# Performance work log

Hardware: AMD Instinct MI355X
Metric: run time of the kernel (lower is better)

Reference implementation:

```python
import jax, jax.numpy as jnp
import numpy as np

NUM_TOKENS = 2048
HIDDEN = 1024
INTER = 2048
NUM_EXPERTS = 8
TOPK = 2


def setup_inputs() -> dict:
    key = jax.random.key(0)
    k1, k2, k3, k4 = jax.random.split(key, 4)
    hidden_states = jax.random.normal(k1, (NUM_TOKENS, HIDDEN), dtype=jnp.float32)
    router_logits = jax.random.normal(k2, (NUM_TOKENS, NUM_EXPERTS), dtype=jnp.float32)
    # fc1: [E, hidden, 2*intermediate] (proj/gate for SwiGLU), fc2: [E, intermediate, hidden]
    w1 = jax.random.normal(k3, (NUM_EXPERTS, HIDDEN, 2 * INTER), dtype=jnp.float32) * 0.02
    w2 = jax.random.normal(k4, (NUM_EXPERTS, INTER, HIDDEN), dtype=jnp.float32) * 0.02
    return {"hidden_states": hidden_states, "router_logits": router_logits, "w1": w1, "w2": w2}


def _grouped_gemm(x, w, expert_ids):
    """x: [T, D], w: [E, D, O], expert_ids: [T] -> [T, O].
    Tokens are routed to expert expert_ids[t]; equivalent to the sequential
    per-expert GEMM on contiguously sorted tokens. Small fixed loop over E."""
    out = jnp.zeros((x.shape[0], w.shape[-1]), dtype=x.dtype)
    for e in range(w.shape[0]):
        mask = (expert_ids == e)[:, None]
        out = out + jnp.where(mask, x, 0.0) @ w[e]
    return out


def reference(hidden_states, router_logits, w1, w2):
    # top-k routing + softmax over the selected logits
    top_logits, top_idx = jax.lax.top_k(router_logits, TOPK)      # [N, K]
    scores = jax.nn.softmax(top_logits, axis=-1)                  # [N, K]

    flat_idx = top_idx.reshape(-1)                                # [N*K]
    sorted_indices = jnp.argsort(flat_idx)                        # permute tokens grouped by expert
    permuted = hidden_states[sorted_indices // TOPK]              # [N*K, D]
    sorted_experts = flat_idx[sorted_indices]                     # [N*K] expert id per permuted row

    fc1_out = _grouped_gemm(permuted, w1, sorted_experts)         # [N*K, 2*I]
    proj, gate = jnp.split(fc1_out, 2, axis=-1)
    act = jax.nn.silu(proj) * gate                                # SwiGLU
    expert_out = _grouped_gemm(act, w2, sorted_experts)           # [N*K, D]

    # unpermute (scatter back) and weighted combine over top-k
    unpermuted = jnp.zeros_like(expert_out).at[sorted_indices].set(expert_out)
    unpermuted = unpermuted.reshape(-1, TOPK, expert_out.shape[-1])
    return (unpermuted * scores[..., None]).sum(axis=1)           # [N, D]
```

## Files before the change

### kernel.cpp

```cpp
#include <hip/hip_runtime.h>
#include <hip/hip_bf16.h>

constexpr int T = 2048;
constexpr int H = 1024;
constexpr int I = 2048;
constexpr int N2 = 2 * I;
constexpr int RCAP = 5120;
constexpr int MAXT = 40;

constexpr int WS_OFF = 16;
constexpr int WS_TEXP = 32;
constexpr int WS_TOPKP = 4256;
constexpr int WS_ROWTOK = 8352;
constexpr int WS_TOKROW = 13472;
constexpr size_t WSB_ZROW = 114688;
constexpr size_t WSB_HSB  = 131072;
constexpr size_t WSB_ACT  = 8u << 20;
constexpr size_t WSB_PW1  = 32u << 20;
constexpr size_t WSB_PW2  = 96u << 20;

constexpr int PW1_BLKS = 8192;
constexpr int PW2_BLKS = 4096;
constexpr int HSB_BLKS = T * H / 2048;
constexpr int FC1_BLKS = 32 * MAXT;

typedef __attribute__((ext_vector_type(4))) float f32x4;
typedef __attribute__((ext_vector_type(8))) short s16x8;

__device__ __forceinline__ short f2bf(float f) {
    unsigned u = __float_as_uint(f);
    u += 0x7FFFu + ((u >> 16) & 1u);
    return (short)(u >> 16);
}

#define MFMA16(a, b, c) __builtin_amdgcn_mfma_f32_16x16x32_bf16(a, b, c, 0, 0, 0)

__device__ __forceinline__ void gl2lds16(const void* g, void* l) {
    __builtin_amdgcn_global_load_lds(
        (const __attribute__((address_space(1))) void*)g,
        (__attribute__((address_space(3))) void*)l, 16, 0, 0);
}

__global__ __launch_bounds__(256) void routing_kernel(const float* __restrict__ logits,
                                                      int* __restrict__ wsi,
                                                      float* __restrict__ wsf) {
    __shared__ int cnt[8], base[9], fill[8];
    const int t = threadIdx.x;
    if (t < 8) { cnt[t] = 0; fill[t] = 0; }
    for (int r = t; r < RCAP; r += 256) wsi[WS_ROWTOK + r] = -1;
    unsigned short* zr = (unsigned short*)((char*)wsi + WSB_ZROW);
    for (int i = t; i < H; i += 256) zr[i] = 0;
    __syncthreads();

    int e0a[8], e1a[8];
    #pragma unroll
    for (int j = 0; j < 8; j++) {
        int tok = t * 8 + j;
        const float* l = logits + tok * 8;
        float v0 = -1e30f; int i0 = 0;
        #pragma unroll
        for (int i = 0; i < 8; i++) { float v = l[i]; if (v > v0) { v0 = v; i0 = i; } }
        float v1 = -1e30f; int i1 = 0;
        #pragma unroll
        for (int i = 0; i < 8; i++) { if (i == i0) continue; float v = l[i]; if (v > v1) { v1 = v; i1 = i; } }
        float ex = __expf(v1 - v0);
        float inv = 1.f / (1.f + ex);
        wsf[WS_TOPKP + tok * 2] = inv;
        wsf[WS_TOPKP + tok * 2 + 1] = ex * inv;
        e0a[j] = i0; e1a[j] = i1;
        atomicAdd(&cnt[i0], 1);
        atomicAdd(&cnt[i1], 1);
    }
    __syncthreads();
    if (t == 0) {
        int acc = 0;
        for (int e = 0; e < 8; e++) { base[e] = acc; acc += (cnt[e] + 127) & ~127; }
        base[8] = acc;
        for (int e = 0; e < 9; e++) wsi[WS_OFF + e] = base[e];
    }
    __syncthreads();
    for (int tt = t; tt < MAXT; tt += 256) {
        int rb = tt * 128, ex = 0;
        for (int e = 0; e < 8; e++)
            if (rb >= base[e] && rb < base[e + 1]) ex = e;
        wsi[WS_TEXP + tt] = ex;
    }
    #pragma unroll
    for (int j = 0; j < 8; j++) {
        int tok = t * 8 + j;
        int ee[2] = {e0a[j], e1a[j]};
        #pragma unroll
        for (int k = 0; k < 2; k++) {
            int e = ee[k];
            int slot = atomicAdd(&fill[e], 1);
            int r = base[e] + slot;
            wsi[WS_ROWTOK + r] = tok;
            wsi[WS_TOKROW + tok * 2 + k] = r;
        }
    }
}

__global__ __launch_bounds__(256) void prep_kernel(
    const float* __restrict__ w1, unsigned short* __restrict__ pw1,
    const float* __restrict__ w2, unsigned short* __restrict__ pw2,
    const float* __restrict__ hs, unsigned short* __restrict__ hsb) {
    const int t = threadIdx.x;
    if (blockIdx.x < PW1_BLKS) {
        int b = blockIdx.x;
        int k0i = b & 31, ct = (b >> 5) & 31, e = b >> 10;
        const float* src = w1 + (size_t)e * H * N2;
        unsigned short* dst = pw1 + (size_t)b * 4096;
        #pragma unroll
        for (int j = 0; j < 2; j++) {
            int g = t + j * 256;
            int kg = g >> 7, n = g & 127;
            int sub = n >> 5, within = n & 31;
            int col = ((sub & 1) ? I : 0) + ct * 64 + (sub >> 1) * 32 + within;
            int kbase = k0i * 32 + kg * 8;
            const float* sp = src + (size_t)kbase * N2 + col;
            s16x8 s;
            #pragma unroll
            for (int kk = 0; kk < 8; kk++) s[kk] = f2bf(sp[(size_t)kk * N2]);
            *(s16x8*)(dst + g * 8) = s;
        }
    } else if (blockIdx.x < PW1_BLKS + PW2_BLKS) {
        int b = blockIdx.x - PW1_BLKS;
        int k0i = b & 63, ht = (b >> 6) & 7, e = b >> 9;
        const float* src = w2 + (size_t)e * I * H;
        unsigned short* dst = pw2 + (size_t)b * 4096;
        #pragma unroll
        for (int j = 0; j < 2; j++) {
            int g = t + j * 256;
            int kg = g >> 7, n = g & 127;
            int col = ht * 128 + n;
            int kbase = k0i * 32 + kg * 8;
            const float* sp = src + (size_t)kbase * H + col;
            s16x8 s;
            #pragma unroll
            for (int kk = 0; kk < 8; kk++) s[kk] = f2bf(sp[(size_t)kk * H]);
            *(s16x8*)(dst + g * 8) = s;
        }
    } else {
        int i = ((blockIdx.x - PW1_BLKS - PW2_BLKS) * 256 + t) * 8;
        f32x4 a = *(const f32x4*)(hs + i);
        f32x4 b = *(const f32x4*)(hs + i + 4);
        s16x8 s = {f2bf(a[0]), f2bf(a[1]), f2bf(a[2]), f2bf(a[3]),
                   f2bf(b[0]), f2bf(b[1]), f2bf(b[2]), f2bf(b[3])};
        *(s16x8*)(hsb + i) = s;
    }
}

__global__ __launch_bounds__(256, 2) void fc1_kernel(
    const unsigned short* __restrict__ hsb, const unsigned short* __restrict__ pw1,
    const int* __restrict__ wsi, const unsigned short* __restrict__ zrow,
    unsigned short* __restrict__ act) {
    __shared__ __align__(16) unsigned short Al[512 * 8];
    __shared__ __align__(16) unsigned short Bl[512 * 8];
    const int t = threadIdx.x;
    const int ct = blockIdx.x & 31, rt = blockIdx.x >> 5;
    const int rowb = rt * 128;
    if (rowb >= wsi[WS_OFF + 8]) return;
    const int e = wsi[WS_TEXP + rt];
    const unsigned short* pb = pw1 + (size_t)((e * 32 + ct) * 32) * 4096;

    const int m = t & 127;
    const int tok = wsi[WS_ROWTOK + rowb + m];
    const unsigned short* rp = (tok >= 0) ? (hsb + (size_t)tok * H) : zrow;
    const int kga = t >> 7;

    const int lane = t & 63, w = t >> 6, wr = w >> 1, wc = w & 1;
    const int q = lane >> 4, l16 = lane & 15;

    f32x4 zero = {0.f, 0.f, 0.f, 0.f};
    f32x4 acc[4][4];
    #pragma unroll
    for (int mi = 0; mi < 4; mi++)
        #pragma unroll
        for (int ni = 0; ni < 4; ni++) acc[mi][ni] = zero;

    for (int k0i = 0; k0i < 32; k0i++) {
        const int k0 = k0i * 32;
        gl2lds16(rp + k0 + kga * 8, &Al[t * 8]);
        gl2lds16(rp + k0 + (kga + 2) * 8, &Al[(t + 256) * 8]);
        const unsigned short* ps = pb + (size_t)k0i * 4096;
        gl2lds16(ps + t * 8, &Bl[t * 8]);
        gl2lds16(ps + (t + 256) * 8, &Bl[(t + 256) * 8]);
        __syncthreads();

        s16x8 af[4], bf[4];
        #pragma unroll
        for (int mi = 0; mi < 4; mi++)
            af[mi] = *(const s16x8*)&Al[(q * 128 + wr * 64 + mi * 16 + l16) * 8];
        #pragma unroll
        for (int ni = 0; ni < 4; ni++)
            bf[ni] = *(const s16x8*)&Bl[(q * 128 + wc * 64 + ni * 16 + l16) * 8];
        #pragma unroll
        for (int mi = 0; mi < 4; mi++)
            #pragma unroll
            for (int ni = 0; ni < 4; ni++)
                acc[mi][ni] = MFMA16(af[mi], bf[ni], acc[mi][ni]);
        __syncthreads();
    }

    #pragma unroll
    for (int mi = 0; mi < 4; mi++)
        #pragma unroll
        for (int r = 0; r < 4; r++) {
            int row = rowb + wr * 64 + mi * 16 + q * 4 + r;
            #pragma unroll
            for (int ni = 0; ni < 2; ni++) {
                int col = ct * 64 + wc * 32 + ni * 16 + l16;
                float p = acc[mi][ni][r], g = acc[mi][ni + 2][r];
                float val = p * g / (1.f + __expf(-p));
                act[(size_t)row * I + col] = (unsigned short)f2bf(val);
            }
        }
}

__global__ __launch_bounds__(256, 2) void fc2_kernel(
    const unsigned short* __restrict__ act, const unsigned short* __restrict__ pw2,
    const int* __restrict__ wsi, float* __restrict__ eo) {
    __shared__ __align__(16) unsigned short Al[512 * 8];
    __shared__ __align__(16) unsigned short Bl[512 * 8];
    const int t = threadIdx.x;
    const int ht = blockIdx.x, rt = blockIdx.y, ks = blockIdx.z;
    const int rowb = rt * 128;
    if (rowb >= wsi[WS_OFF + 8]) return;
    const int e = wsi[WS_TEXP + rt];
    const unsigned short* pb = pw2 + (size_t)((e * 8 + ht) * 64) * 4096;

    const int m = t & 127;
    const unsigned short* rp = act + (size_t)(rowb + m) * I;
    const int kga = t >> 7;

    const int lane = t & 63, w = t >> 6, wr = w >> 1, wc = w & 1;
    const int q = lane >> 4, l16 = lane & 15;

    f32x4 zero = {0.f, 0.f, 0.f, 0.f};
    f32x4 acc[4][4];
    #pragma unroll
    for (int mi = 0; mi < 4; mi++)
        #pragma unroll
        for (int ni = 0; ni < 4; ni++) acc[mi][ni] = zero;

    for (int k0i = ks * 32; k0i < ks * 32 + 32; k0i++) {
        const int k0 = k0i * 32;
        gl2lds16(rp + k0 + kga * 8, &Al[t * 8]);
        gl2lds16(rp + k0 + (kga + 2) * 8, &Al[(t + 256) * 8]);
        const unsigned short* ps = pb + (size_t)k0i * 4096;
        gl2lds16(ps + t * 8, &Bl[t * 8]);
        gl2lds16(ps + (t + 256) * 8, &Bl[(t + 256) * 8]);
        __syncthreads();

        s16x8 af[4], bf[4];
        #pragma unroll
        for (int mi = 0; mi < 4; mi++)
            af[mi] = *(const s16x8*)&Al[(q * 128 + wr * 64 + mi * 16 + l16) * 8];
        #pragma unroll
        for (int ni = 0; ni < 4; ni++)
            bf[ni] = *(const s16x8*)&Bl[(q * 128 + wc * 64 + ni * 16 + l16) * 8];
        #pragma unroll
        for (int mi = 0; mi < 4; mi++)
            #pragma unroll
            for (int ni = 0; ni < 4; ni++)
                acc[mi][ni] = MFMA16(af[mi], bf[ni], acc[mi][ni]);
        __syncthreads();
    }

    float* ed = eo + (size_t)ks * RCAP * H;
    #pragma unroll
    for (int mi = 0; mi < 4; mi++)
        #pragma unroll
        for (int r = 0; r < 4; r++) {
            int row = rowb + wr * 64 + mi * 16 + q * 4 + r;
            #pragma unroll
            for (int ni = 0; ni < 4; ni++) {
                int col = ht * 128 + wc * 64 + ni * 16 + l16;
                ed[(size_t)row * H + col] = acc[mi][ni][r];
            }
        }
}

__global__ __launch_bounds__(256) void combine_kernel(
    const float* __restrict__ eo, const int* __restrict__ wsi,
    const float* __restrict__ wsf, float* __restrict__ out) {
    const int tok = blockIdx.x;
    const int r0 = wsi[WS_TOKROW + tok * 2], r1 = wsi[WS_TOKROW + tok * 2 + 1];
    const float s0 = wsf[WS_TOPKP + tok * 2], s1 = wsf[WS_TOPKP + tok * 2 + 1];
    const float* a0 = eo + (size_t)r0 * H;
    const float* a1 = eo + (size_t)RCAP * H + (size_t)r0 * H;
    const float* b0 = eo + (size_t)r1 * H;
    const float* b1 = eo + (size_t)RCAP * H + (size_t)r1 * H;
    const int c = threadIdx.x * 4;
    f32x4 va0 = *(const f32x4*)(a0 + c), va1 = *(const f32x4*)(a1 + c);
    f32x4 vb0 = *(const f32x4*)(b0 + c), vb1 = *(const f32x4*)(b1 + c);
    f32x4 r;
    #pragma unroll
    for (int i = 0; i < 4; i++) r[i] = s0 * (va0[i] + va1[i]) + s1 * (vb0[i] + vb1[i]);
    *(f32x4*)(out + (size_t)tok * H + c) = r;
}

extern "C" void kernel_launch(void* const* d_in, const int* in_sizes, int n_in,
                              void* d_out, int out_size, void* d_ws, size_t ws_size,
                              hipStream_t stream) {
    const float* hs     = (const float*)d_in[0];
    const float* logits = (const float*)d_in[1];
    const float* w1     = (const float*)d_in[2];
    const float* w2     = (const float*)d_in[3];
    float* out = (float*)d_out;
    int* wsi = (int*)d_ws;
    float* wsf = (float*)d_ws;
    unsigned short* zrow = (unsigned short*)((char*)d_ws + WSB_ZROW);
    unsigned short* hsb  = (unsigned short*)((char*)d_ws + WSB_HSB);
    unsigned short* act  = (unsigned short*)((char*)d_ws + WSB_ACT);
    unsigned short* pw1  = (unsigned short*)((char*)d_ws + WSB_PW1);
    unsigned short* pw2  = (unsigned short*)((char*)d_ws + WSB_PW2);
    float* eo = (float*)((char*)d_ws + WSB_PW1);

    routing_kernel<<<1, 256, 0, stream>>>(logits, wsi, wsf);
    prep_kernel<<<PW1_BLKS + PW2_BLKS + HSB_BLKS, 256, 0, stream>>>(w1, pw1, w2, pw2, hs, hsb);
    fc1_kernel<<<FC1_BLKS, 256, 0, stream>>>(hsb, pw1, wsi, zrow, act);
    fc2_kernel<<<dim3(8, MAXT, 2), 256, 0, stream>>>(act, pw2, wsi, eo);
    combine_kernel<<<T, 256, 0, stream>>>(eo, wsi, wsf, out);
}
```

Baseline: 382.3 us.

## Coalesce weight prep via LDS transpose, deterministic routing prefix sums, raise GEMM occupancy

```diff
diff --git a/kernel.cpp b/kernel.cpp
--- a/kernel.cpp
+++ b/kernel.cpp
@@ -19,13 +19,14 @@
 constexpr size_t WSB_PW1  = 32u << 20;
 constexpr size_t WSB_PW2  = 96u << 20;
 
-constexpr int PW1_BLKS = 8192;
-constexpr int PW2_BLKS = 4096;
+constexpr int PW1_BLKS = 2048;
+constexpr int PW2_BLKS = 2048;
 constexpr int HSB_BLKS = T * H / 2048;
 constexpr int FC1_BLKS = 32 * MAXT;
 
 typedef __attribute__((ext_vector_type(4))) float f32x4;
 typedef __attribute__((ext_vector_type(8))) short s16x8;
+typedef __attribute__((ext_vector_type(4))) short s16x4;
 
 __device__ __forceinline__ short f2bf(float f) {
     unsigned u = __float_as_uint(f);
@@ -44,15 +45,16 @@
 __global__ __launch_bounds__(256) void routing_kernel(const float* __restrict__ logits,
                                                       int* __restrict__ wsi,
                                                       float* __restrict__ wsf) {
-    __shared__ int cnt[8], base[9], fill[8];
+    __shared__ unsigned char lds_e[T * 2];
+    __shared__ int pre[8][257];
+    __shared__ int base[9];
     const int t = threadIdx.x;
-    if (t < 8) { cnt[t] = 0; fill[t] = 0; }
+
     for (int r = t; r < RCAP; r += 256) wsi[WS_ROWTOK + r] = -1;
     unsigned short* zr = (unsigned short*)((char*)wsi + WSB_ZROW);
     for (int i = t; i < H; i += 256) zr[i] = 0;
-    __syncthreads();
-
-    int e0a[8], e1a[8];
+
+    unsigned long long cnt = 0;
     #pragma unroll
     for (int j = 0; j < 8; j++) {
         int tok = t * 8 + j;
@@ -67,14 +69,22 @@
         float inv = 1.f / (1.f + ex);
         wsf[WS_TOPKP + tok * 2] = inv;
         wsf[WS_TOPKP + tok * 2 + 1] = ex * inv;
-        e0a[j] = i0; e1a[j] = i1;
-        atomicAdd(&cnt[i0], 1);
-        atomicAdd(&cnt[i1], 1);
+        lds_e[tok * 2] = (unsigned char)i0;
+        lds_e[tok * 2 + 1] = (unsigned char)i1;
+        cnt += 1ull << (i0 * 8);
+        cnt += 1ull << (i1 * 8);
+    }
+    #pragma unroll
+    for (int e = 0; e < 8; e++) pre[e][t + 1] = (int)((cnt >> (e * 8)) & 0xff);
+    __syncthreads();
+    if (t < 8) {
+        int s = 0; pre[t][0] = 0;
+        for (int i = 1; i <= 256; i++) { s += pre[t][i]; pre[t][i] = s; }
     }
     __syncthreads();
     if (t == 0) {
         int acc = 0;
-        for (int e = 0; e < 8; e++) { base[e] = acc; acc += (cnt[e] + 127) & ~127; }
+        for (int e = 0; e < 8; e++) { base[e] = acc; acc += (pre[e][256] + 127) & ~127; }
         base[8] = acc;
         for (int e = 0; e < 9; e++) wsi[WS_OFF + e] = base[e];
     }
@@ -85,15 +95,15 @@
             if (rb >= base[e] && rb < base[e + 1]) ex = e;
         wsi[WS_TEXP + tt] = ex;
     }
+    unsigned long long run = 0;
     #pragma unroll
     for (int j = 0; j < 8; j++) {
         int tok = t * 8 + j;
-        int ee[2] = {e0a[j], e1a[j]};
         #pragma unroll
         for (int k = 0; k < 2; k++) {
-            int e = ee[k];
-            int slot = atomicAdd(&fill[e], 1);
-            int r = base[e] + slot;
+            int e = lds_e[tok * 2 + k];
+            int r = base[e] + pre[e][t] + (int)((run >> (e * 8)) & 0xff);
+            run += 1ull << (e * 8);
             wsi[WS_ROWTOK + r] = tok;
             wsi[WS_TOKROW + tok * 2 + k] = r;
         }
@@ -104,41 +114,57 @@
     const float* __restrict__ w1, unsigned short* __restrict__ pw1,
     const float* __restrict__ w2, unsigned short* __restrict__ pw2,
     const float* __restrict__ hs, unsigned short* __restrict__ hsb) {
+    __shared__ __align__(16) short L[8 * 2048];
     const int t = threadIdx.x;
+
     if (blockIdx.x < PW1_BLKS) {
         int b = blockIdx.x;
-        int k0i = b & 31, ct = (b >> 5) & 31, e = b >> 10;
-        const float* src = w1 + (size_t)e * H * N2;
-        unsigned short* dst = pw1 + (size_t)b * 4096;
-        #pragma unroll
-        for (int j = 0; j < 2; j++) {
-            int g = t + j * 256;
-            int kg = g >> 7, n = g & 127;
-            int sub = n >> 5, within = n & 31;
-            int col = ((sub & 1) ? I : 0) + ct * 64 + (sub >> 1) * 32 + within;
-            int kbase = k0i * 32 + kg * 8;
-            const float* sp = src + (size_t)kbase * N2 + col;
-            s16x8 s;
-            #pragma unroll
-            for (int kk = 0; kk < 8; kk++) s[kk] = f2bf(sp[(size_t)kk * N2]);
-            *(s16x8*)(dst + g * 8) = s;
+        int ch = b & 1, kd = (b >> 1) & 127, e = b >> 8;
+        const float* s0 = w1 + (size_t)e * H * N2 + (size_t)(kd * 8) * N2 + ch * I;
+        #pragma unroll
+        for (int j = 0; j < 16; j++) {
+            int cc = j * 256 + t;
+            int r = cc >> 9, cx = cc & 511;
+            f32x4 v = *(const f32x4*)(s0 + (size_t)r * N2 + cx * 4);
+            s16x4 s = {f2bf(v[0]), f2bf(v[1]), f2bf(v[2]), f2bf(v[3])};
+            *(s16x4*)&L[r * 2048 + cx * 4] = s;
+        }
+        __syncthreads();
+        const int k0i = kd >> 2, kg = kd & 3;
+        #pragma unroll
+        for (int j = 0; j < 8; j++) {
+            int u = j * 256 + t;
+            int ct = u >> 6, nh = u & 63;
+            int sh = nh >> 5, within = nh & 31;
+            int n = (sh * 2 + ch) * 32 + within;
+            int cl = ct * 64 + sh * 32 + within;
+            s16x8 o;
+            #pragma unroll
+            for (int kk = 0; kk < 8; kk++) o[kk] = L[kk * 2048 + cl];
+            *(s16x8*)(pw1 + (size_t)((e * 32 + ct) * 32 + k0i) * 4096 + kg * 1024 + n * 8) = o;
         }
     } else if (blockIdx.x < PW1_BLKS + PW2_BLKS) {
         int b = blockIdx.x - PW1_BLKS;
-        int k0i = b & 63, ht = (b >> 6) & 7, e = b >> 9;
-        const float* src = w2 + (size_t)e * I * H;
-        unsigned short* dst = pw2 + (size_t)b * 4096;
-        #pragma unroll
-        for (int j = 0; j < 2; j++) {
-            int g = t + j * 256;
-            int kg = g >> 7, n = g & 127;
-            int col = ht * 128 + n;
-            int kbase = k0i * 32 + kg * 8;
-            const float* sp = src + (size_t)kbase * H + col;
-            s16x8 s;
-            #pragma unroll
-            for (int kk = 0; kk < 8; kk++) s[kk] = f2bf(sp[(size_t)kk * H]);
-            *(s16x8*)(dst + g * 8) = s;
+        int kd = b & 255, e = b >> 8;
+        const float* s0 = w2 + (size_t)e * I * H + (size_t)(kd * 8) * H;
+        #pragma unroll
+        for (int j = 0; j < 8; j++) {
+            int cc = j * 256 + t;
+            f32x4 v = *(const f32x4*)(s0 + cc * 4);
+            int r = cc >> 8, cx = cc & 255;
+            s16x4 s = {f2bf(v[0]), f2bf(v[1]), f2bf(v[2]), f2bf(v[3])};
+            *(s16x4*)&L[r * 1024 + cx * 4] = s;
+        }
+        __syncthreads();
+        const int k0i = kd >> 2, kg = kd & 3;
+        #pragma unroll
+        for (int j = 0; j < 4; j++) {
+            int u = j * 256 + t;
+            int ht = u >> 7, n = u & 127;
+            s16x8 o;
+            #pragma unroll
+            for (int kk = 0; kk < 8; kk++) o[kk] = L[kk * 1024 + u];
+            *(s16x8*)(pw2 + (size_t)((e * 8 + ht) * 64 + k0i) * 4096 + kg * 1024 + n * 8) = o;
         }
     } else {
         int i = ((blockIdx.x - PW1_BLKS - PW2_BLKS) * 256 + t) * 8;
@@ -150,7 +176,7 @@
     }
 }
 
-__global__ __launch_bounds__(256, 2) void fc1_kernel(
+__global__ __launch_bounds__(256, 4) void fc1_kernel(
     const unsigned short* __restrict__ hsb, const unsigned short* __restrict__ pw1,
     const int* __restrict__ wsi, const unsigned short* __restrict__ zrow,
     unsigned short* __restrict__ act) {
@@ -217,7 +243,7 @@
         }
 }
 
-__global__ __launch_bounds__(256, 2) void fc2_kernel(
+__global__ __launch_bounds__(256, 4) void fc2_kernel(
     const unsigned short* __restrict__ act, const unsigned short* __restrict__ pw2,
     const int* __restrict__ wsi, float* __restrict__ eo) {
     __shared__ __align__(16) unsigned short Al[512 * 8];
```

Measured after the change: 386.9 us. No clear change (+1.2%).
